# Kernel tuning notes

Hardware: AMD Instinct MI355X
Metric: run time of the kernel (lower is better)

The kernel has to match this reference:

```python
import jax, jax.numpy as jnp
import numpy as np

B, S, IN, OUT = 8, 2048, 1024, 4096
QMAX = 255.0  # 2**8 - 1 levels for 8-bit


def _quantize(x):
    """Per-tensor affine int8 quantization, matching Int8Linear.quantize."""
    x_max = x.max()
    x_min = x.min()
    scale = (x_max - x_min) / QMAX
    zero_point = jnp.round((x_max * -128.0 - x_min * 127.0) / (x_max - x_min))
    # torch does .to(torch.int8): wrapping cast; round has zero grad, int cast detaches
    x_q = jax.lax.stop_gradient((jnp.round(x / scale) + zero_point).astype(jnp.int8))
    return x_q, scale, zero_point


def setup_inputs() -> dict:
    key = jax.random.key(0)
    kx, kw, kb = jax.random.split(key, 3)
    x = jax.random.normal(kx, (B, S, IN), dtype=jnp.float32)
    w = jax.random.normal(kw, (OUT, IN), dtype=jnp.float32) * 0.02  # nn.Linear-ish init scale
    w_q, w_scale, w_zp = _quantize(w)  # done once at module init in torch
    bias = jax.random.normal(kb, (OUT,), dtype=jnp.float32) * 0.01
    return {
        "x": x,
        "w_q": w_q.astype(jnp.int32),  # stored int8 values, carried as int32
        "w_scale": w_scale,
        "w_zp": w_zp,
        "bias": bias,
    }


def reference(x, w_q, w_scale, w_zp, bias):
    # quantize activation per call (per-tensor affine)
    x_q, x_scale, x_zp = _quantize(x)
    # torch: matmul(x_q.to(int32) - x_zero_point, weight.T.to(int32) - zero_point)
    # zero points are FLOAT tensors, so the subtraction promotes to float32 and the
    # GEMM runs in float32 on centered integer-valued operands.
    xc = x_q.astype(jnp.float32) - x_zp            # [B, S, IN]
    wc = w_q.astype(jnp.float32) - w_zp            # [OUT, IN]
    acc = jnp.einsum('bsi,oi->bso', xc, wc)        # [B, S, OUT]
    return acc * (x_scale * w_scale) + bias
```

## Files before the change

### kernel.cpp

```cpp
#include <hip/hip_runtime.h>
#include <stdint.h>

#define M_ROWS 16384
#define N_COLS 4096
#define K_DIM  1024
#define NT     (K_DIM / 128)

typedef int   i32x4 __attribute__((ext_vector_type(4)));
typedef float f32x4 __attribute__((ext_vector_type(4)));

__device__ __forceinline__ void gload_lds16(const void* g, void* l) {
    __builtin_amdgcn_global_load_lds(
        (const __attribute__((address_space(1))) unsigned int*)g,
        (__attribute__((address_space(3))) unsigned int*)l, 16, 0, 0);
}

#define SBAR() do { __builtin_amdgcn_sched_barrier(0); \
                    __builtin_amdgcn_s_barrier();      \
                    __builtin_amdgcn_sched_barrier(0); } while (0)

__global__ void k_minmax(const float4* __restrict__ x,
                         float* __restrict__ pmax, float* __restrict__ pmin) {
    const int n4 = (M_ROWS * K_DIM) / 4;
    float mx = -3.402823466e38f, mn = 3.402823466e38f;
    for (int i = blockIdx.x * blockDim.x + threadIdx.x; i < n4;
         i += gridDim.x * blockDim.x) {
        float4 v = x[i];
        mx = fmaxf(mx, fmaxf(fmaxf(v.x, v.y), fmaxf(v.z, v.w)));
        mn = fminf(mn, fminf(fminf(v.x, v.y), fminf(v.z, v.w)));
    }
#pragma unroll
    for (int off = 32; off > 0; off >>= 1) {
        mx = fmaxf(mx, __shfl_xor(mx, off));
        mn = fminf(mn, __shfl_xor(mn, off));
    }
    __shared__ float smx[4], smn[4];
    const int wave = threadIdx.x >> 6, lane = threadIdx.x & 63;
    if (lane == 0) { smx[wave] = mx; smn[wave] = mn; }
    __syncthreads();
    if (threadIdx.x == 0) {
        mx = fmaxf(fmaxf(smx[0], smx[1]), fmaxf(smx[2], smx[3]));
        mn = fminf(fminf(smn[0], smn[1]), fminf(smn[2], smn[3]));
        pmax[blockIdx.x] = mx;
        pmin[blockIdx.x] = mn;
    }
}

__global__ void k_scalars(const float* __restrict__ pmax, const float* __restrict__ pmin,
                          const float* __restrict__ w_scale, float* __restrict__ scal) {
    float mx = -3.402823466e38f, mn = 3.402823466e38f;
    for (int i = threadIdx.x; i < 2048; i += 256) {
        mx = fmaxf(mx, pmax[i]);
        mn = fminf(mn, pmin[i]);
    }
#pragma unroll
    for (int off = 32; off > 0; off >>= 1) {
        mx = fmaxf(mx, __shfl_xor(mx, off));
        mn = fminf(mn, __shfl_xor(mn, off));
    }
    __shared__ float smx[4], smn[4];
    const int wave = threadIdx.x >> 6, lane = threadIdx.x & 63;
    if (lane == 0) { smx[wave] = mx; smn[wave] = mn; }
    __syncthreads();
    if (threadIdx.x == 0) {
        mx = fmaxf(fmaxf(smx[0], smx[1]), fmaxf(smx[2], smx[3]));
        mn = fminf(fminf(smn[0], smn[1]), fminf(smn[2], smn[3]));
        const float scale = (mx - mn) / 255.0f;
        const float zp = rintf((mx * -128.0f - mn * 127.0f) / (mx - mn));
        scal[0] = scale;
        scal[1] = zp;
        scal[2] = scale * w_scale[0];
    }
}

__global__ void k_quant(const float* __restrict__ x, const float* __restrict__ scal,
                        const float* __restrict__ wzp,
                        int4* __restrict__ xc8, float* __restrict__ cm) {
    const float scale = scal[0], zx = scal[1], zw = wzp[0];
    const int lane = threadIdx.x & 63;
    const int gw = (blockIdx.x * blockDim.x + threadIdx.x) >> 6;
    const int nw = (gridDim.x * blockDim.x) >> 6;
    for (int row = gw; row < M_ROWS; row += nw) {
        const float4* xr = (const float4*)(x + (size_t)row * K_DIM + lane * 16);
        union { signed char c[16]; int4 v; } u;
        int s = 0;
#pragma unroll
        for (int e = 0; e < 4; ++e) {
            float4 v = xr[e];
            signed char c0 = (signed char)(int)(rintf(v.x / scale) + zx);
            signed char c1 = (signed char)(int)(rintf(v.y / scale) + zx);
            signed char c2 = (signed char)(int)(rintf(v.z / scale) + zx);
            signed char c3 = (signed char)(int)(rintf(v.w / scale) + zx);
            u.c[e * 4 + 0] = c0; u.c[e * 4 + 1] = c1;
            u.c[e * 4 + 2] = c2; u.c[e * 4 + 3] = c3;
            s += (int)c0 + (int)c1 + (int)c2 + (int)c3;
        }
        xc8[row * 64 + lane] = u.v;
#pragma unroll
        for (int off = 32; off > 0; off >>= 1) s += __shfl_xor(s, off);
        if (lane == 0) cm[row] = zw * (1024.0f * zx - (float)s);
    }
}

__global__ void k_prepw(const int* __restrict__ wq, const float* __restrict__ scal,
                        int4* __restrict__ wc8, float* __restrict__ cn) {
    const float zx = scal[1];
    const int lane = threadIdx.x & 63;
    const int gw = (blockIdx.x * blockDim.x + threadIdx.x) >> 6;
    const int nw = (gridDim.x * blockDim.x) >> 6;
    for (int row = gw; row < N_COLS; row += nw) {
        const int4* wr = (const int4*)(wq + (size_t)row * K_DIM + lane * 16);
        union { signed char c[16]; int4 v; } u;
        int s = 0;
#pragma unroll
        for (int e = 0; e < 4; ++e) {
            int4 v = wr[e];
            u.c[e * 4 + 0] = (signed char)v.x;
            u.c[e * 4 + 1] = (signed char)v.y;
            u.c[e * 4 + 2] = (signed char)v.z;
            u.c[e * 4 + 3] = (signed char)v.w;
            s += v.x + v.y + v.z + v.w;
        }
        wc8[row * 64 + lane] = u.v;
#pragma unroll
        for (int off = 32; off > 0; off >>= 1) s += __shfl_xor(s, off);
        if (lane == 0) cn[row] = -zx * (float)s;
    }
}

__global__ __launch_bounds__(512, 2)
void k_gemm(const signed char* __restrict__ A,
            const signed char* __restrict__ B,
            const float* __restrict__ scal,
            const float* __restrict__ bias,
            const float* __restrict__ cm,
            const float* __restrict__ cn,
            float* __restrict__ C) {
    __shared__ char lds[131072];

    const int tid  = threadIdx.x;
    const int wave = tid >> 6, lane = tid & 63;
    const int wm = wave >> 2, wn = wave & 3;
    const int fr = lane & 15, kg = lane >> 4;

    const int wg  = blockIdx.x;
    const int swz = ((wg & 7) << 7) | (wg >> 3);
    const int bm  = swz >> 4;
    const int bn  = swz & 15;

    const int scol = ((tid & 7) ^ ((tid >> 3) & 7)) << 4;
    const char* gA = (const char*)A + (size_t)(bm * 256 + (tid >> 3)) * K_DIM + scol;
    const char* gB = (const char*)B + (size_t)(bn * 256 + (tid >> 3)) * K_DIM + scol;

#define STAGE_A(tt, h, b) do {                                           \
        const char* g_ = gA + (size_t)(tt) * 128 + (size_t)(h) * 131072; \
        char* l_ = lds + (b) * 32768 + (h) * 16384 + wave * 1024;        \
        gload_lds16(g_, l_);                                             \
        gload_lds16(g_ + 65536, l_ + 8192);                              \
    } while (0)
#define STAGE_B(tt, h, b) do {                                           \
        const char* g_ = gB + (size_t)(tt) * 128 + (size_t)(h) * 131072; \
        char* l_ = lds + 65536 + (b) * 32768 + (h) * 16384 + wave * 1024; \
        gload_lds16(g_, l_);                                             \
        gload_lds16(g_ + 65536, l_ + 8192);                              \
    } while (0)

    const int kx0 = ((kg * 16) ^ ((fr & 7) << 4));
    const int kx1 = ((64 + kg * 16) ^ ((fr & 7) << 4));
    const int arow = (wm * 128 + fr) * 128;
    const int brow = (wn * 64 + fr) * 128;

    i32x4 acc[8][4] = {};
    i32x4 bf[4][2];

    STAGE_A(0, 0, 0); STAGE_A(0, 1, 0);
    STAGE_B(0, 0, 0); STAGE_B(0, 1, 0);
    STAGE_B(1, 0, 1); STAGE_B(1, 1, 1);
    asm volatile("s_waitcnt vmcnt(4)" ::: "memory");
    SBAR();

    for (int t = 0; t < NT; ++t) {
        const int b = t & 1;
        const char* Ab = lds + b * 32768;
        const char* Bb = lds + 65536 + b * 32768;
#pragma unroll
        for (int q = 0; q < 4; ++q) {
            i32x4 af[2][2];
            if (q == 0) {
#pragma unroll
                for (int j = 0; j < 4; ++j) {
                    bf[j][0] = *(const i32x4*)(Bb + brow + j * 2048 + kx0);
                    bf[j][1] = *(const i32x4*)(Bb + brow + j * 2048 + kx1);
                }
            }
#pragma unroll
            for (int i2 = 0; i2 < 2; ++i2) {
                const int i = 2 * q + i2;
                af[i2][0] = *(const i32x4*)(Ab + arow + i * 2048 + kx0);
                af[i2][1] = *(const i32x4*)(Ab + arow + i * 2048 + kx1);
            }
            if (q == 0)      { if (t + 1 < NT) STAGE_A(t + 1, 0, b ^ 1); }
            else if (q == 1) { if (t + 1 < NT) STAGE_A(t + 1, 1, b ^ 1); }
            else if (q == 2) { if (t + 2 < NT) STAGE_B(t + 2, 0, b); }
            else {
                if (t + 2 < NT) {
                    STAGE_B(t + 2, 1, b);
                    asm volatile("s_waitcnt vmcnt(4)" ::: "memory");
                } else {
                    asm volatile("s_waitcnt vmcnt(0)" ::: "memory");
                }
            }
            SBAR();
            __builtin_amdgcn_s_setprio(1);
#pragma unroll
            for (int kk = 0; kk < 2; ++kk)
#pragma unroll
                for (int i2 = 0; i2 < 2; ++i2)
#pragma unroll
                    for (int j = 0; j < 4; ++j)
                        acc[2 * q + i2][j] = __builtin_amdgcn_mfma_i32_16x16x64_i8(
                            af[i2][kk], bf[j][kk], acc[2 * q + i2][j], 0, 0, 0);
            __builtin_amdgcn_s_setprio(0);
            SBAR();
        }
    }

    const float alpha = scal[2];
    const int gc_base = bn * 256 + wn * 64;
    const int gr_base = bm * 256 + wm * 128;
    float bb[4], cc[4];
#pragma unroll
    for (int j = 0; j < 4; ++j) {
        const int gc = gc_base + j * 16 + fr;
        bb[j] = bias[gc];
        cc[j] = cn[gc];
    }
#pragma unroll
    for (int i = 0; i < 8; ++i) {
        const int gr0 = gr_base + i * 16 + kg * 4;
        const float4 cmv = *(const float4*)(cm + gr0);
#pragma unroll
        for (int j = 0; j < 4; ++j) {
            const int gc = gc_base + j * 16 + fr;
            C[(size_t)(gr0 + 0) * N_COLS + gc] = ((float)acc[i][j][0] + cmv.x + cc[j]) * alpha + bb[j];
            C[(size_t)(gr0 + 1) * N_COLS + gc] = ((float)acc[i][j][1] + cmv.y + cc[j]) * alpha + bb[j];
            C[(size_t)(gr0 + 2) * N_COLS + gc] = ((float)acc[i][j][2] + cmv.z + cc[j]) * alpha + bb[j];
            C[(size_t)(gr0 + 3) * N_COLS + gc] = ((float)acc[i][j][3] + cmv.w + cc[j]) * alpha + bb[j];
        }
    }
#undef STAGE_A
#undef STAGE_B
}

extern "C" void kernel_launch(void* const* d_in, const int* in_sizes, int n_in,
                              void* d_out, int out_size, void* d_ws, size_t ws_size,
                              hipStream_t stream) {
    const float* x    = (const float*)d_in[0];
    const int*   wq   = (const int*)d_in[1];
    const float* wsc  = (const float*)d_in[2];
    const float* wzp  = (const float*)d_in[3];
    const float* bias = (const float*)d_in[4];
    float* out = (float*)d_out;

    char* ws = (char*)d_ws;
    int4*  xc8  = (int4*)(ws);
    int4*  wc8  = (int4*)(ws + 16777216);
    float* cm   = (float*)(ws + 20971520);
    float* cn   = (float*)(ws + 21037056);
    float* pmax = (float*)(ws + 21053440);
    float* pmin = (float*)(ws + 21061632);
    float* scal = (float*)(ws + 21069824);

    k_minmax <<<2048, 256, 0, stream>>>((const float4*)x, pmax, pmin);
    k_scalars<<<1,    256, 0, stream>>>(pmax, pmin, wsc, scal);
    k_prepw  <<<1024, 256, 0, stream>>>(wq, scal, wc8, cn);
    k_quant  <<<2048, 256, 0, stream>>>(x, scal, wzp, xc8, cm);
    k_gemm   <<<1024, 512, 0, stream>>>((const signed char*)xc8, (const signed char*)wc8,
                                        scal, bias, cm, cn, out);
}
```

Baseline: 407.4 us.

## Replace pipelined 256x256 int8 GEMM with simple 128x128 single-buffered tiles

Rewrites the GEMM kernel to use 128x128 output tiles with 256 threads and 4096 blocks, loading each 128-wide K slice into a 32KB LDS buffer and syncing before and after the MFMA loop. It removes the double-buffered prefetch schedule, priority hints and 128KB LDS footprint in favor of higher occupancy and simpler code. It risks exposing global load latency and increasing operand reloads from smaller tiles.

```diff
diff --git a/kernel.cpp b/kernel.cpp
--- a/kernel.cpp
+++ b/kernel.cpp
@@ -7,17 +7,12 @@
 #define NT     (K_DIM / 128)
 
 typedef int   i32x4 __attribute__((ext_vector_type(4)));
-typedef float f32x4 __attribute__((ext_vector_type(4)));
 
 __device__ __forceinline__ void gload_lds16(const void* g, void* l) {
     __builtin_amdgcn_global_load_lds(
         (const __attribute__((address_space(1))) unsigned int*)g,
         (__attribute__((address_space(3))) unsigned int*)l, 16, 0, 0);
 }
-
-#define SBAR() do { __builtin_amdgcn_sched_barrier(0); \
-                    __builtin_amdgcn_s_barrier();      \
-                    __builtin_amdgcn_sched_barrier(0); } while (0)
 
 __global__ void k_minmax(const float4* __restrict__ x,
                          float* __restrict__ pmax, float* __restrict__ pmin) {
@@ -128,7 +123,7 @@
     }
 }
 
-__global__ __launch_bounds__(512, 2)
+__global__ __launch_bounds__(256, 3)
 void k_gemm(const signed char* __restrict__ A,
             const signed char* __restrict__ B,
             const float* __restrict__ scal,
@@ -136,98 +131,60 @@
             const float* __restrict__ cm,
             const float* __restrict__ cn,
             float* __restrict__ C) {
-    __shared__ char lds[131072];
+    __shared__ char lds[32768];
 
     const int tid  = threadIdx.x;
     const int wave = tid >> 6, lane = tid & 63;
-    const int wm = wave >> 2, wn = wave & 3;
+    const int wm = wave >> 1, wn = wave & 1;
     const int fr = lane & 15, kg = lane >> 4;
 
     const int wg  = blockIdx.x;
-    const int swz = ((wg & 7) << 7) | (wg >> 3);
-    const int bm  = swz >> 4;
-    const int bn  = swz & 15;
+    const int swz = ((wg & 7) << 9) | (wg >> 3);
+    const int bm  = swz >> 5;
+    const int bn  = swz & 31;
 
     const int scol = ((tid & 7) ^ ((tid >> 3) & 7)) << 4;
-    const char* gA = (const char*)A + (size_t)(bm * 256 + (tid >> 3)) * K_DIM + scol;
-    const char* gB = (const char*)B + (size_t)(bn * 256 + (tid >> 3)) * K_DIM + scol;
-
-#define STAGE_A(tt, h, b) do {                                           \
-        const char* g_ = gA + (size_t)(tt) * 128 + (size_t)(h) * 131072; \
-        char* l_ = lds + (b) * 32768 + (h) * 16384 + wave * 1024;        \
-        gload_lds16(g_, l_);                                             \
-        gload_lds16(g_ + 65536, l_ + 8192);                              \
-    } while (0)
-#define STAGE_B(tt, h, b) do {                                           \
-        const char* g_ = gB + (size_t)(tt) * 128 + (size_t)(h) * 131072; \
-        char* l_ = lds + 65536 + (b) * 32768 + (h) * 16384 + wave * 1024; \
-        gload_lds16(g_, l_);                                             \
-        gload_lds16(g_ + 65536, l_ + 8192);                              \
-    } while (0)
+    const char* gA = (const char*)A + (size_t)(bm * 128 + (tid >> 3)) * K_DIM + scol;
+    const char* gB = (const char*)B + (size_t)(bn * 128 + (tid >> 3)) * K_DIM + scol;
 
     const int kx0 = ((kg * 16) ^ ((fr & 7) << 4));
     const int kx1 = ((64 + kg * 16) ^ ((fr & 7) << 4));
-    const int arow = (wm * 128 + fr) * 128;
+    const int arow = (wm * 64 + fr) * 128;
     const int brow = (wn * 64 + fr) * 128;
 
-    i32x4 acc[8][4] = {};
-    i32x4 bf[4][2];
-
-    STAGE_A(0, 0, 0); STAGE_A(0, 1, 0);
-    STAGE_B(0, 0, 0); STAGE_B(0, 1, 0);
-    STAGE_B(1, 0, 1); STAGE_B(1, 1, 1);
-    asm volatile("s_waitcnt vmcnt(4)" ::: "memory");
-    SBAR();
+    i32x4 acc[4][4] = {};
 
     for (int t = 0; t < NT; ++t) {
-        const int b = t & 1;
-        const char* Ab = lds + b * 32768;
-        const char* Bb = lds + 65536 + b * 32768;
-#pragma unroll
-        for (int q = 0; q < 4; ++q) {
-            i32x4 af[2][2];
-            if (q == 0) {
-#pragma unroll
-                for (int j = 0; j < 4; ++j) {
-                    bf[j][0] = *(const i32x4*)(Bb + brow + j * 2048 + kx0);
-                    bf[j][1] = *(const i32x4*)(Bb + brow + j * 2048 + kx1);
-                }
-            }
-#pragma unroll
-            for (int i2 = 0; i2 < 2; ++i2) {
-                const int i = 2 * q + i2;
-                af[i2][0] = *(const i32x4*)(Ab + arow + i * 2048 + kx0);
-                af[i2][1] = *(const i32x4*)(Ab + arow + i * 2048 + kx1);
-            }
-            if (q == 0)      { if (t + 1 < NT) STAGE_A(t + 1, 0, b ^ 1); }
-            else if (q == 1) { if (t + 1 < NT) STAGE_A(t + 1, 1, b ^ 1); }
-            else if (q == 2) { if (t + 2 < NT) STAGE_B(t + 2, 0, b); }
-            else {
-                if (t + 2 < NT) {
-                    STAGE_B(t + 2, 1, b);
-                    asm volatile("s_waitcnt vmcnt(4)" ::: "memory");
-                } else {
-                    asm volatile("s_waitcnt vmcnt(0)" ::: "memory");
-                }
-            }
-            SBAR();
-            __builtin_amdgcn_s_setprio(1);
-#pragma unroll
-            for (int kk = 0; kk < 2; ++kk)
-#pragma unroll
-                for (int i2 = 0; i2 < 2; ++i2)
-#pragma unroll
-                    for (int j = 0; j < 4; ++j)
-                        acc[2 * q + i2][j] = __builtin_amdgcn_mfma_i32_16x16x64_i8(
-                            af[i2][kk], bf[j][kk], acc[2 * q + i2][j], 0, 0, 0);
-            __builtin_amdgcn_s_setprio(0);
-            SBAR();
-        }
+#pragma unroll
+        for (int h = 0; h < 4; ++h) {
+            const size_t goff = (size_t)t * 128 + (size_t)h * 32 * 1024;
+            gload_lds16(gA + goff, lds + h * 4096 + wave * 1024);
+            gload_lds16(gB + goff, lds + 16384 + h * 4096 + wave * 1024);
+        }
+        __syncthreads();
+
+        i32x4 af[4][2], bf[4][2];
+#pragma unroll
+        for (int i = 0; i < 4; ++i) {
+            af[i][0] = *(const i32x4*)(lds + arow + i * 2048 + kx0);
+            af[i][1] = *(const i32x4*)(lds + arow + i * 2048 + kx1);
+            bf[i][0] = *(const i32x4*)(lds + 16384 + brow + i * 2048 + kx0);
+            bf[i][1] = *(const i32x4*)(lds + 16384 + brow + i * 2048 + kx1);
+        }
+#pragma unroll
+        for (int kk = 0; kk < 2; ++kk)
+#pragma unroll
+            for (int i = 0; i < 4; ++i)
+#pragma unroll
+                for (int j = 0; j < 4; ++j)
+                    acc[i][j] = __builtin_amdgcn_mfma_i32_16x16x64_i8(
+                        af[i][kk], bf[j][kk], acc[i][j], 0, 0, 0);
+        __syncthreads();
     }
 
     const float alpha = scal[2];
-    const int gc_base = bn * 256 + wn * 64;
-    const int gr_base = bm * 256 + wm * 128;
+    const int gc_base = bn * 128 + wn * 64;
+    const int gr_base = bm * 128 + wm * 64;
     float bb[4], cc[4];
 #pragma unroll
     for (int j = 0; j < 4; ++j) {
@@ -236,7 +193,7 @@
         cc[j] = cn[gc];
     }
 #pragma unroll
-    for (int i = 0; i < 8; ++i) {
+    for (int i = 0; i < 4; ++i) {
         const int gr0 = gr_base + i * 16 + kg * 4;
         const float4 cmv = *(const float4*)(cm + gr0);
 #pragma unroll
@@ -248,8 +205,6 @@
             C[(size_t)(gr0 + 3) * N_COLS + gc] = ((float)acc[i][j][3] + cmv.w + cc[j]) * alpha + bb[j];
         }
     }
-#undef STAGE_A
-#undef STAGE_B
 }
 
 extern "C" void kernel_launch(void* const* d_in, const int* in_sizes, int n_in,
@@ -275,6 +230,6 @@
     k_scalars<<<1,    256, 0, stream>>>(pmax, pmin, wsc, scal);
     k_prepw  <<<1024, 256, 0, stream>>>(wq, scal, wc8, cn);
     k_quant  <<<2048, 256, 0, stream>>>(x, scal, wzp, xc8, cm);
-    k_gemm   <<<1024, 512, 0, stream>>>((const signed char*)xc8, (const signed char*)wc8,
+    k_gemm   <<<4096, 256, 0, stream>>>((const signed char*)xc8, (const signed char*)wc8,
                                         scal, bias, cm, cn, out);
 }
```

New measurement: 412.4 us. Within noise of the previous version (+1.2%).

## Make GEMM persistent over four N tiles per workgroup with fused epilogue constants

Applied to the files above, without the earlier changes.

The GEMM grid shrinks from 1024 to 256 workgroups. Each workgroup keeps one 256-row A block and walks four consecutive 256-column B blocks in a single pipelined loop, writing its output and zeroing the accumulators after each block. The row and column correction terms are pre-multiplied by alpha, with bias folded into the column term in the prep kernels, which removes work from the epilogue. The aim is to cut per-workgroup prologue costs and keep the pipeline flowing across tiles. The costs are a grid of only 256 workgroups against 256 CUs at two-wave occupancy, and epilogue stores that now stall the loop in the middle of the pipeline.

```diff
diff --git a/kernel.cpp b/kernel.cpp
--- a/kernel.cpp
+++ b/kernel.cpp
@@ -4,10 +4,9 @@
 #define M_ROWS 16384
 #define N_COLS 4096
 #define K_DIM  1024
-#define NT     (K_DIM / 128)
-
-typedef int   i32x4 __attribute__((ext_vector_type(4)));
-typedef float f32x4 __attribute__((ext_vector_type(4)));
+#define NTILES 32
+
+typedef int i32x4 __attribute__((ext_vector_type(4)));
 
 __device__ __forceinline__ void gload_lds16(const void* g, void* l) {
     __builtin_amdgcn_global_load_lds(
@@ -75,8 +74,8 @@
 
 __global__ void k_quant(const float* __restrict__ x, const float* __restrict__ scal,
                         const float* __restrict__ wzp,
-                        int4* __restrict__ xc8, float* __restrict__ cm) {
-    const float scale = scal[0], zx = scal[1], zw = wzp[0];
+                        int4* __restrict__ xc8, float* __restrict__ cma) {
+    const float scale = scal[0], zx = scal[1], zw = wzp[0], alpha = scal[2];
     const int lane = threadIdx.x & 63;
     const int gw = (blockIdx.x * blockDim.x + threadIdx.x) >> 6;
     const int nw = (gridDim.x * blockDim.x) >> 6;
@@ -98,13 +97,14 @@
         xc8[row * 64 + lane] = u.v;
 #pragma unroll
         for (int off = 32; off > 0; off >>= 1) s += __shfl_xor(s, off);
-        if (lane == 0) cm[row] = zw * (1024.0f * zx - (float)s);
+        if (lane == 0) cma[row] = zw * (1024.0f * zx - (float)s) * alpha;
     }
 }
 
 __global__ void k_prepw(const int* __restrict__ wq, const float* __restrict__ scal,
-                        int4* __restrict__ wc8, float* __restrict__ cn) {
-    const float zx = scal[1];
+                        const float* __restrict__ bias,
+                        int4* __restrict__ wc8, float* __restrict__ cnb) {
+    const float zx = scal[1], alpha = scal[2];
     const int lane = threadIdx.x & 63;
     const int gw = (blockIdx.x * blockDim.x + threadIdx.x) >> 6;
     const int nw = (gridDim.x * blockDim.x) >> 6;
@@ -124,7 +124,7 @@
         wc8[row * 64 + lane] = u.v;
 #pragma unroll
         for (int off = 32; off > 0; off >>= 1) s += __shfl_xor(s, off);
-        if (lane == 0) cn[row] = -zx * (float)s;
+        if (lane == 0) cnb[row] = -zx * (float)s * alpha + bias[row];
     }
 }
 
@@ -132,9 +132,8 @@
 void k_gemm(const signed char* __restrict__ A,
             const signed char* __restrict__ B,
             const float* __restrict__ scal,
-            const float* __restrict__ bias,
-            const float* __restrict__ cm,
-            const float* __restrict__ cn,
+            const float* __restrict__ cma,
+            const float* __restrict__ cnb,
             float* __restrict__ C) {
     __shared__ char lds[131072];
 
@@ -143,26 +142,27 @@
     const int wm = wave >> 2, wn = wave & 3;
     const int fr = lane & 15, kg = lane >> 4;
 
-    const int wg  = blockIdx.x;
-    const int swz = ((wg & 7) << 7) | (wg >> 3);
-    const int bm  = swz >> 4;
-    const int bn  = swz & 15;
+    const int blk   = blockIdx.x;
+    const int bm    = (blk & 7) * 8 + (blk >> 5);
+    const int bngrp = (blk >> 3) & 3;
 
     const int scol = ((tid & 7) ^ ((tid >> 3) & 7)) << 4;
-    const char* gA = (const char*)A + (size_t)(bm * 256 + (tid >> 3)) * K_DIM + scol;
-    const char* gB = (const char*)B + (size_t)(bn * 256 + (tid >> 3)) * K_DIM + scol;
-
-#define STAGE_A(tt, h, b) do {                                           \
-        const char* g_ = gA + (size_t)(tt) * 128 + (size_t)(h) * 131072; \
-        char* l_ = lds + (b) * 32768 + (h) * 16384 + wave * 1024;        \
-        gload_lds16(g_, l_);                                             \
-        gload_lds16(g_ + 65536, l_ + 8192);                              \
+    const int srow = tid >> 3;
+    const char* gA  = (const char*)A + (size_t)(bm * 256 + srow) * K_DIM + scol;
+    const char* gB0 = (const char*)B + (size_t)(bngrp * 4 * 256 + srow) * K_DIM + scol;
+
+#define STAGE_A(u, h) do {                                                    \
+        const char* g_ = gA + (size_t)((u) & 7) * 128 + (size_t)(h) * 131072; \
+        char* l_ = lds + ((u) & 1) * 32768 + (h) * 16384 + wave * 1024;       \
+        gload_lds16(g_, l_);                                                  \
+        gload_lds16(g_ + 65536, l_ + 8192);                                   \
     } while (0)
-#define STAGE_B(tt, h, b) do {                                           \
-        const char* g_ = gB + (size_t)(tt) * 128 + (size_t)(h) * 131072; \
-        char* l_ = lds + 65536 + (b) * 32768 + (h) * 16384 + wave * 1024; \
-        gload_lds16(g_, l_);                                             \
-        gload_lds16(g_ + 65536, l_ + 8192);                              \
+#define STAGE_B(u, h) do {                                                    \
+        const char* g_ = gB0 + (size_t)((u) >> 3) * 262144                    \
+                             + (size_t)((u) & 7) * 128 + (size_t)(h) * 131072; \
+        char* l_ = lds + 65536 + ((u) & 1) * 32768 + (h) * 16384 + wave * 1024; \
+        gload_lds16(g_, l_);                                                  \
+        gload_lds16(g_ + 65536, l_ + 8192);                                   \
     } while (0)
 
     const int kx0 = ((kg * 16) ^ ((fr & 7) << 4));
@@ -170,17 +170,19 @@
     const int arow = (wm * 128 + fr) * 128;
     const int brow = (wn * 64 + fr) * 128;
 
+    const float alpha = scal[2];
+
     i32x4 acc[8][4] = {};
     i32x4 bf[4][2];
 
-    STAGE_A(0, 0, 0); STAGE_A(0, 1, 0);
-    STAGE_B(0, 0, 0); STAGE_B(0, 1, 0);
-    STAGE_B(1, 0, 1); STAGE_B(1, 1, 1);
+    STAGE_A(0, 0); STAGE_A(0, 1);
+    STAGE_B(0, 0); STAGE_B(0, 1);
+    STAGE_B(1, 0); STAGE_B(1, 1);
     asm volatile("s_waitcnt vmcnt(4)" ::: "memory");
     SBAR();
 
-    for (int t = 0; t < NT; ++t) {
-        const int b = t & 1;
+    for (int u = 0; u < NTILES; ++u) {
+        const int b = u & 1;
         const char* Ab = lds + b * 32768;
         const char* Bb = lds + 65536 + b * 32768;
 #pragma unroll
@@ -199,12 +201,12 @@
                 af[i2][0] = *(const i32x4*)(Ab + arow + i * 2048 + kx0);
                 af[i2][1] = *(const i32x4*)(Ab + arow + i * 2048 + kx1);
             }
-            if (q == 0)      { if (t + 1 < NT) STAGE_A(t + 1, 0, b ^ 1); }
-            else if (q == 1) { if (t + 1 < NT) STAGE_A(t + 1, 1, b ^ 1); }
-            else if (q == 2) { if (t + 2 < NT) STAGE_B(t + 2, 0, b); }
+            if (q == 0)      { if (u + 1 < NTILES) STAGE_A(u + 1, 0); }
+            else if (q == 1) { if (u + 1 < NTILES) STAGE_A(u + 1, 1); }
+            else if (q == 2) { if (u + 2 < NTILES) STAGE_B(u + 2, 0); }
             else {
-                if (t + 2 < NT) {
-                    STAGE_B(t + 2, 1, b);
+                if (u + 2 < NTILES) {
+                    STAGE_B(u + 2, 1);
                     asm volatile("s_waitcnt vmcnt(4)" ::: "memory");
                 } else {
                     asm volatile("s_waitcnt vmcnt(0)" ::: "memory");
@@ -223,29 +225,32 @@
             __builtin_amdgcn_s_setprio(0);
             SBAR();
         }
-    }
-
-    const float alpha = scal[2];
-    const int gc_base = bn * 256 + wn * 64;
-    const int gr_base = bm * 256 + wm * 128;
-    float bb[4], cc[4];
-#pragma unroll
-    for (int j = 0; j < 4; ++j) {
-        const int gc = gc_base + j * 16 + fr;
-        bb[j] = bias[gc];
-        cc[j] = cn[gc];
-    }
-#pragma unroll
-    for (int i = 0; i < 8; ++i) {
-        const int gr0 = gr_base + i * 16 + kg * 4;
-        const float4 cmv = *(const float4*)(cm + gr0);
-#pragma unroll
-        for (int j = 0; j < 4; ++j) {
-            const int gc = gc_base + j * 16 + fr;
-            C[(size_t)(gr0 + 0) * N_COLS + gc] = ((float)acc[i][j][0] + cmv.x + cc[j]) * alpha + bb[j];
-            C[(size_t)(gr0 + 1) * N_COLS + gc] = ((float)acc[i][j][1] + cmv.y + cc[j]) * alpha + bb[j];
-            C[(size_t)(gr0 + 2) * N_COLS + gc] = ((float)acc[i][j][2] + cmv.z + cc[j]) * alpha + bb[j];
-            C[(size_t)(gr0 + 3) * N_COLS + gc] = ((float)acc[i][j][3] + cmv.w + cc[j]) * alpha + bb[j];
+
+        if ((u & 7) == 7) {
+            const int g = u >> 3;
+            const int gc_base = (bngrp * 4 + g) * 256 + wn * 64;
+            const int gr_base = bm * 256 + wm * 128;
+            float cc[4];
+#pragma unroll
+            for (int j = 0; j < 4; ++j) cc[j] = cnb[gc_base + j * 16 + fr];
+#pragma unroll
+            for (int i = 0; i < 8; ++i) {
+                const int gr0 = gr_base + i * 16 + kg * 4;
+                const float4 cmv = *(const float4*)(cma + gr0);
+#pragma unroll
+                for (int j = 0; j < 4; ++j) {
+                    const int gc = gc_base + j * 16 + fr;
+                    C[(size_t)(gr0 + 0) * N_COLS + gc] = (float)acc[i][j][0] * alpha + (cmv.x + cc[j]);
+                    C[(size_t)(gr0 + 1) * N_COLS + gc] = (float)acc[i][j][1] * alpha + (cmv.y + cc[j]);
+                    C[(size_t)(gr0 + 2) * N_COLS + gc] = (float)acc[i][j][2] * alpha + (cmv.z + cc[j]);
+                    C[(size_t)(gr0 + 3) * N_COLS + gc] = (float)acc[i][j][3] * alpha + (cmv.w + cc[j]);
+                }
+            }
+#pragma unroll
+            for (int i = 0; i < 8; ++i)
+#pragma unroll
+                for (int j = 0; j < 4; ++j)
+                    acc[i][j] = (i32x4){0, 0, 0, 0};
         }
     }
 #undef STAGE_A
@@ -265,16 +270,16 @@
     char* ws = (char*)d_ws;
     int4*  xc8  = (int4*)(ws);
     int4*  wc8  = (int4*)(ws + 16777216);
-    float* cm   = (float*)(ws + 20971520);
-    float* cn   = (float*)(ws + 21037056);
+    float* cma  = (float*)(ws + 20971520);
+    float* cnb  = (float*)(ws + 21037056);
     float* pmax = (float*)(ws + 21053440);
     float* pmin = (float*)(ws + 21061632);
     float* scal = (float*)(ws + 21069824);
 
     k_minmax <<<2048, 256, 0, stream>>>((const float4*)x, pmax, pmin);
     k_scalars<<<1,    256, 0, stream>>>(pmax, pmin, wsc, scal);
-    k_prepw  <<<1024, 256, 0, stream>>>(wq, scal, wc8, cn);
-    k_quant  <<<2048, 256, 0, stream>>>(x, scal, wzp, xc8, cm);
-    k_gemm   <<<1024, 512, 0, stream>>>((const signed char*)xc8, (const signed char*)wc8,
-                                        scal, bias, cm, cn, out);
-}
+    k_prepw  <<<1024, 256, 0, stream>>>(wq, scal, bias, wc8, cnb);
+    k_quant  <<<2048, 256, 0, stream>>>(x, scal, wzp, xc8, cma);
+    k_gemm   <<<256,  512, 0, stream>>>((const signed char*)xc8, (const signed char*)wc8,
+                                        scal, cma, cnb, out);
+}
```

After: 427.5 us. 4.9% more time.
